# Kernel tuning notes

Hardware: AMD Instinct MI355X
Metric: run time of the kernel (lower is better)

## Reference

```python
import jax, jax.numpy as jnp
import numpy as np

N = 10000  # num_users + num_posts


def gcn_conv(x, edge_index, W, b):
    """PyG-style GCNConv: out = D^-1/2 (A+I) D^-1/2 (x W) + b."""
    h = x @ W  # [N, d]
    src, dst = edge_index[0], edge_index[1]
    loop = jnp.arange(N, dtype=src.dtype)
    src = jnp.concatenate([src, loop])
    dst = jnp.concatenate([dst, loop])
    ones = jnp.ones(src.shape[0], dtype=h.dtype)
    deg = jax.ops.segment_sum(ones, dst, num_segments=N)  # in-degree incl. self-loop
    dinv = jnp.where(deg > 0, jax.lax.rsqrt(deg), 0.0)
    norm = dinv[src] * dinv[dst]  # [E+N]
    msg = h[src] * norm[:, None]  # gather + scale
    out = jax.ops.segment_sum(msg, dst, num_segments=N)  # scatter-add
    return out + b


def setup_inputs() -> dict:
    key = jax.random.key(0)
    k1, k2, k3, k4 = jax.random.split(key, 4)
    E = 320000
    H = 64
    x = jax.random.normal(k1, (N, N), dtype=jnp.float32)
    edge_index = jax.random.randint(k2, (2, E), 0, N, dtype=jnp.int64)
    W1 = jax.random.normal(k3, (N, H), dtype=jnp.float32) / np.sqrt(N)
    b1 = jnp.zeros((H,), dtype=jnp.float32)
    W2 = jax.random.normal(k4, (H, H), dtype=jnp.float32) / np.sqrt(H)
    b2 = jnp.zeros((H,), dtype=jnp.float32)
    return {"x": x, "edge_index": edge_index, "W1": W1, "b1": b1, "W2": W2, "b2": b2}


def reference(x, edge_index, W1, b1, W2, b2):
    h = gcn_conv(x, edge_index, W1, b1)
    h = jax.nn.relu(h)
    return gcn_conv(h, edge_index, W2, b2)
```

## Files before the change

### kernel.cpp

```cpp
#include <hip/hip_runtime.h>
#include <hip/hip_bf16.h>

#define NND 10000
#define HD 64
#define KPAD 10112
#define ROWS 64
#define RBLK 157
#define NCHUNK 3
#define KCHUNK 3456
#define KSTEP 128
#define KHEAD 5632
#define CAP 96
#define ABYTES 32768
#define BBYTES 16384
#define BUFB (ABYTES + BBYTES)

typedef __attribute__((ext_vector_type(8))) short bf16x8;
typedef __attribute__((ext_vector_type(4))) float f32x4;

__device__ __forceinline__ short f2bf(float f) {
    unsigned u = __builtin_bit_cast(unsigned, f);
    u += 0x7FFFu + ((u >> 16) & 1u);
    return (short)(u >> 16);
}

__device__ __forceinline__ void gload16(const void* gp, void* lp) {
    __builtin_amdgcn_global_load_lds(
        (const __attribute__((address_space(1))) unsigned int*)gp,
        (__attribute__((address_space(3))) unsigned int*)lp, 16, 0, 0);
}

__device__ __forceinline__ void gload16nt(const void* gp, void* lp) {
    __builtin_amdgcn_global_load_lds(
        (const __attribute__((address_space(1))) unsigned int*)gp,
        (__attribute__((address_space(3))) unsigned int*)lp, 16, 0, 2);
}

__global__ __launch_bounds__(256) void prep2_kernel(const float* __restrict__ W1,
        int* __restrict__ cnt, float* __restrict__ h, short* __restrict__ w1t) {
    __shared__ float tile[64][65];
    const int t = threadIdx.x;
    const int k0 = blockIdx.x * 64;
    #pragma unroll
    for (int i = 0; i < 16; ++i) {
        int r = i * 4 + (t >> 6);
        int c = t & 63;
        int k = k0 + r;
        tile[r][c] = (k < NND) ? W1[(size_t)k * HD + c] : 0.f;
    }
    __syncthreads();
    #pragma unroll
    for (int i = 0; i < 16; ++i) {
        int c = i * 4 + (t >> 6);
        int k = t & 63;
        if (k0 + k < KPAD)
            w1t[(size_t)c * KPAD + k0 + k] = f2bf(tile[k][c]);
    }
    int tid = blockIdx.x * 256 + t;
    if (tid < NND) cnt[tid] = 0;
    f32x4* h4 = (f32x4*)h;
    f32x4 z = {0.f, 0.f, 0.f, 0.f};
    #pragma unroll
    for (int i = 0; i < 4; ++i) {
        int idx = tid + i * 40448;
        if (idx < NND * HD / 4) h4[idx] = z;
    }
}

__global__ __launch_bounds__(256, 1) void csrgemm1_kernel(const float* __restrict__ x,
        const short* __restrict__ w1t, float* __restrict__ h,
        const int* __restrict__ ei, int* __restrict__ cnt, int* __restrict__ csr, int E) {
    {
        const int stride = RBLK * NCHUNK * 256;
        for (int e = blockIdx.x * 256 + threadIdx.x; e < E; e += stride) {
            int s = ei[e], d = ei[E + e];
            int pos = atomicAdd(&cnt[d], 1);
            if (pos < CAP) csr[d * CAP + pos] = s;
        }
    }
    asm volatile("s_waitcnt vmcnt(0)" ::: "memory");
    __shared__ f32x4 smem4[3 * BUFB / 16];
    char* smem = (char*)smem4;
    const int l = threadIdx.x & 63;
    const int w = threadIdx.x >> 6;
    const int r0 = (blockIdx.x / NCHUNK) * ROWS;
    const int kstart = (blockIdx.x % NCHUNK) * KCHUNK;
    const int kend = min(KPAD, kstart + KCHUNK);
    const int nsteps = (kend - kstart) >> 7;

    const int wr = (w & 1) * 32;
    const int wc = (w >> 1) * 32;
    const int akg = l >> 4;
    const int l15 = l & 15;
    const int l7 = l & 7;

    f32x4 acc[2][2];
    #pragma unroll
    for (int i = 0; i < 2; ++i)
        #pragma unroll
        for (int j = 0; j < 2; ++j) acc[i][j] = f32x4{0.f, 0.f, 0.f, 0.f};

    union AFU { bf16x8 v; __hip_bfloat162 p[4]; };

    auto stage = [&](int buf, int k0) {
        char* sb = smem + buf * BUFB;
        const bool cached = (k0 < KHEAD);
        #pragma unroll
        for (int i = 0; i < 8; ++i) {
            int row = w * 16 + i * 2 + (l >> 5);
            int rg = r0 + row; if (rg >= NND) rg = 0;
            int pl = ((l & 31) >> 1) ^ (row & 7);
            const char* gp = (const char*)x + (size_t)rg * (NND * 4)
                             + (size_t)k0 * 4 + pl * 32 + (l & 1) * 16;
            if (k0 + pl * 8 + (l & 1) * 4 + 3 >= NND)
                gp = (const char*)x;
            if (cached) gload16(gp, sb + w * 8192 + i * 1024);
            else        gload16nt(gp, sb + w * 8192 + i * 1024);
        }
        #pragma unroll
        for (int j = 0; j < 4; ++j) {
            int col = w * 16 + j * 4 + (l >> 4);
            int cl = (l & 15) ^ (col & 7);
            const char* gp = (const char*)w1t + (size_t)col * (KPAD * 2)
                             + (size_t)k0 * 2 + cl * 16;
            gload16(gp, sb + ABYTES + w * 4096 + j * 1024);
        }
    };

    stage(0, kstart);
    if (nsteps > 1) stage(1, kstart + KSTEP);
    for (int t = 0; t < nsteps; ++t) {
        if (t + 1 < nsteps) asm volatile("s_waitcnt vmcnt(12)" ::: "memory");
        else                asm volatile("s_waitcnt vmcnt(0)" ::: "memory");
        __builtin_amdgcn_s_barrier();
        if (t + 2 < nsteps) stage((t + 2) % 3, kstart + (t + 2) * KSTEP);
        const char* sb = smem + (t % 3) * BUFB;
        #pragma unroll
        for (int ks = 0; ks < 4; ++ks) {
            int cp = (ks * 4 + akg) ^ l7;
            #pragma unroll
            for (int rg = 0; rg < 2; ++rg) {
                int arow = wr + rg * 16 + l15;
                const char* ap = sb + arow * 512 + cp * 32;
                f32x4 a0 = *(const f32x4*)ap;
                f32x4 a1 = *(const f32x4*)(ap + 16);
                AFU af;
                af.p[0] = __float22bfloat162_rn(float2{a0[0], a0[1]});
                af.p[1] = __float22bfloat162_rn(float2{a0[2], a0[3]});
                af.p[2] = __float22bfloat162_rn(float2{a1[0], a1[1]});
                af.p[3] = __float22bfloat162_rn(float2{a1[2], a1[3]});
                #pragma unroll
                for (int cg = 0; cg < 2; ++cg) {
                    int col = wc + cg * 16 + l15;
                    bf16x8 b = *(const bf16x8*)(sb + ABYTES + col * 256 + cp * 16);
                    acc[rg][cg] = __builtin_amdgcn_mfma_f32_16x16x32_bf16(af.v, b, acc[rg][cg], 0, 0, 0);
                }
            }
        }
    }
    #pragma unroll
    for (int rg = 0; rg < 2; ++rg) {
        const int crow = r0 + wr + rg * 16 + akg * 4;
        #pragma unroll
        for (int cg = 0; cg < 2; ++cg) {
            const int ccol = wc + cg * 16 + l15;
            #pragma unroll
            for (int j = 0; j < 4; ++j) {
                int row = crow + j;
                if (row < NND)
                    unsafeAtomicAdd(&h[(size_t)row * HD + ccol], acc[rg][cg][j]);
            }
        }
    }
}

__global__ __launch_bounds__(256) void agg1g2_kernel(const float* __restrict__ h,
        const int* __restrict__ csr, const int* __restrict__ cnt,
        const float* __restrict__ b1, const float* __restrict__ W2,
        float* __restrict__ h2) {
    __shared__ float w2s[HD * HD];
    __shared__ float rowbuf[4][HD];
    for (int i = threadIdx.x; i < HD * HD; i += 256) w2s[i] = W2[i];
    const int wave = threadIdx.x >> 6, lane = threadIdx.x & 63;
    const int d = blockIdx.x * 4 + wave;
    const int n = min(cnt[d], CAP);
    const float dd = rsqrtf((float)(n + 1));
    float acc = fmaf(h[(size_t)d * HD + lane], dd * dd, b1[lane]);
    const int* row = csr + d * CAP;
    int j = 0;
    for (; j + 8 <= n; j += 8) {
        int s0 = row[j],   s1 = row[j+1], s2 = row[j+2], s3 = row[j+3];
        int s4 = row[j+4], s5 = row[j+5], s6 = row[j+6], s7 = row[j+7];
        acc = fmaf(h[(size_t)s0 * HD + lane], rsqrtf((float)(cnt[s0] + 1)) * dd, acc);
        acc = fmaf(h[(size_t)s1 * HD + lane], rsqrtf((float)(cnt[s1] + 1)) * dd, acc);
        acc = fmaf(h[(size_t)s2 * HD + lane], rsqrtf((float)(cnt[s2] + 1)) * dd, acc);
        acc = fmaf(h[(size_t)s3 * HD + lane], rsqrtf((float)(cnt[s3] + 1)) * dd, acc);
        acc = fmaf(h[(size_t)s4 * HD + lane], rsqrtf((float)(cnt[s4] + 1)) * dd, acc);
        acc = fmaf(h[(size_t)s5 * HD + lane], rsqrtf((float)(cnt[s5] + 1)) * dd, acc);
        acc = fmaf(h[(size_t)s6 * HD + lane], rsqrtf((float)(cnt[s6] + 1)) * dd, acc);
        acc = fmaf(h[(size_t)s7 * HD + lane], rsqrtf((float)(cnt[s7] + 1)) * dd, acc);
    }
    for (; j < n; ++j) {
        int s0 = row[j];
        acc = fmaf(h[(size_t)s0 * HD + lane], rsqrtf((float)(cnt[s0] + 1)) * dd, acc);
    }
    rowbuf[wave][lane] = fmaxf(acc, 0.f);
    __syncthreads();
    float s = 0.f;
    #pragma unroll
    for (int k = 0; k < HD; ++k)
        s = fmaf(rowbuf[wave][k], w2s[k * HD + lane], s);
    h2[(size_t)d * HD + lane] = s;
}

__global__ __launch_bounds__(256) void agg2_kernel(const float* __restrict__ feat,
        const int* __restrict__ csr, const int* __restrict__ cnt,
        const float* __restrict__ bias, float* __restrict__ out) {
    const int wave = threadIdx.x >> 6, lane = threadIdx.x & 63;
    const int d = blockIdx.x * 4 + wave;
    const int n = min(cnt[d], CAP);
    const float dd = rsqrtf((float)(n + 1));
    float acc = fmaf(feat[(size_t)d * HD + lane], dd * dd, bias[lane]);
    const int* row = csr + d * CAP;
    int j = 0;
    for (; j + 8 <= n; j += 8) {
        int s0 = row[j],   s1 = row[j+1], s2 = row[j+2], s3 = row[j+3];
        int s4 = row[j+4], s5 = row[j+5], s6 = row[j+6], s7 = row[j+7];
        acc = fmaf(feat[(size_t)s0 * HD + lane], rsqrtf((float)(cnt[s0] + 1)) * dd, acc);
        acc = fmaf(feat[(size_t)s1 * HD + lane], rsqrtf((float)(cnt[s1] + 1)) * dd, acc);
        acc = fmaf(feat[(size_t)s2 * HD + lane], rsqrtf((float)(cnt[s2] + 1)) * dd, acc);
        acc = fmaf(feat[(size_t)s3 * HD + lane], rsqrtf((float)(cnt[s3] + 1)) * dd, acc);
        acc = fmaf(feat[(size_t)s4 * HD + lane], rsqrtf((float)(cnt[s4] + 1)) * dd, acc);
        acc = fmaf(feat[(size_t)s5 * HD + lane], rsqrtf((float)(cnt[s5] + 1)) * dd, acc);
        acc = fmaf(feat[(size_t)s6 * HD + lane], rsqrtf((float)(cnt[s6] + 1)) * dd, acc);
        acc = fmaf(feat[(size_t)s7 * HD + lane], rsqrtf((float)(cnt[s7] + 1)) * dd, acc);
    }
    for (; j < n; ++j) {
        int s0 = row[j];
        acc = fmaf(feat[(size_t)s0 * HD + lane], rsqrtf((float)(cnt[s0] + 1)) * dd, acc);
    }
    out[(size_t)d * HD + lane] = acc;
}

extern "C" void kernel_launch(void* const* d_in, const int* in_sizes, int n_in,
                              void* d_out, int out_size, void* d_ws, size_t ws_size,
                              hipStream_t stream) {
    const float* x  = (const float*)d_in[0];
    const int*   ei = (const int*)d_in[1];
    const float* W1 = (const float*)d_in[2];
    const float* b1 = (const float*)d_in[3];
    const float* W2 = (const float*)d_in[4];
    const float* b2 = (const float*)d_in[5];
    float* out = (float*)d_out;
    const int E = in_sizes[1] / 2;

    char* ws = (char*)d_ws;
    int*   cnt  = (int*)(ws);
    float* h    = (float*)(ws + 40000);
    float* h2   = (float*)(ws + 2600000);
    short* w1t  = (short*)(ws + 5160000);
    int*   csr  = (int*)(ws + 6454336);

    prep2_kernel<<<158, 256, 0, stream>>>(W1, cnt, h, w1t);
    csrgemm1_kernel<<<RBLK * NCHUNK, 256, 0, stream>>>(x, w1t, h, ei, cnt, csr, E);
    agg1g2_kernel<<<2500, 256, 0, stream>>>(h, csr, cnt, b1, W2, h2);
    agg2_kernel<<<2500, 256, 0, stream>>>(h2, csr, cnt, b2, out);
}
```

Baseline: 137.1 us.

## Drop split-K in first GEMM, store results directly, overlap CSR build with prefetch

```diff
diff --git a/kernel.cpp b/kernel.cpp
--- a/kernel.cpp
+++ b/kernel.cpp
@@ -6,8 +6,6 @@
 #define KPAD 10112
 #define ROWS 64
 #define RBLK 157
-#define NCHUNK 3
-#define KCHUNK 3456
 #define KSTEP 128
 #define KHEAD 5632
 #define CAP 96
@@ -37,7 +35,7 @@
 }
 
 __global__ __launch_bounds__(256) void prep2_kernel(const float* __restrict__ W1,
-        int* __restrict__ cnt, float* __restrict__ h, short* __restrict__ w1t) {
+        int* __restrict__ cnt, short* __restrict__ w1t) {
     __shared__ float tile[64][65];
     const int t = threadIdx.x;
     const int k0 = blockIdx.x * 64;
@@ -58,35 +56,17 @@
     }
     int tid = blockIdx.x * 256 + t;
     if (tid < NND) cnt[tid] = 0;
-    f32x4* h4 = (f32x4*)h;
-    f32x4 z = {0.f, 0.f, 0.f, 0.f};
-    #pragma unroll
-    for (int i = 0; i < 4; ++i) {
-        int idx = tid + i * 40448;
-        if (idx < NND * HD / 4) h4[idx] = z;
-    }
 }
 
 __global__ __launch_bounds__(256, 1) void csrgemm1_kernel(const float* __restrict__ x,
         const short* __restrict__ w1t, float* __restrict__ h,
         const int* __restrict__ ei, int* __restrict__ cnt, int* __restrict__ csr, int E) {
-    {
-        const int stride = RBLK * NCHUNK * 256;
-        for (int e = blockIdx.x * 256 + threadIdx.x; e < E; e += stride) {
-            int s = ei[e], d = ei[E + e];
-            int pos = atomicAdd(&cnt[d], 1);
-            if (pos < CAP) csr[d * CAP + pos] = s;
-        }
-    }
-    asm volatile("s_waitcnt vmcnt(0)" ::: "memory");
     __shared__ f32x4 smem4[3 * BUFB / 16];
     char* smem = (char*)smem4;
     const int l = threadIdx.x & 63;
     const int w = threadIdx.x >> 6;
-    const int r0 = (blockIdx.x / NCHUNK) * ROWS;
-    const int kstart = (blockIdx.x % NCHUNK) * KCHUNK;
-    const int kend = min(KPAD, kstart + KCHUNK);
-    const int nsteps = (kend - kstart) >> 7;
+    const int r0 = blockIdx.x * ROWS;
+    const int nsteps = KPAD >> 7;
 
     const int wr = (w & 1) * 32;
     const int wc = (w >> 1) * 32;
@@ -127,13 +107,48 @@
         }
     };
 
-    stage(0, kstart);
-    if (nsteps > 1) stage(1, kstart + KSTEP);
+    stage(0, 0);
+    stage(1, KSTEP);
+    {
+        const int tid = blockIdx.x * 256 + threadIdx.x;
+        const int stride8 = RBLK * 256 * 8;
+        for (int base = tid * 8; base < E; base += stride8) {
+            if (base + 8 <= E) {
+                int4 sa = *(const int4*)(ei + base);
+                int4 sb = *(const int4*)(ei + base + 4);
+                int4 da = *(const int4*)(ei + E + base);
+                int4 db = *(const int4*)(ei + E + base + 4);
+                int p0 = atomicAdd(&cnt[da.x], 1);
+                int p1 = atomicAdd(&cnt[da.y], 1);
+                int p2 = atomicAdd(&cnt[da.z], 1);
+                int p3 = atomicAdd(&cnt[da.w], 1);
+                int p4 = atomicAdd(&cnt[db.x], 1);
+                int p5 = atomicAdd(&cnt[db.y], 1);
+                int p6 = atomicAdd(&cnt[db.z], 1);
+                int p7 = atomicAdd(&cnt[db.w], 1);
+                if (p0 < CAP) csr[da.x * CAP + p0] = sa.x;
+                if (p1 < CAP) csr[da.y * CAP + p1] = sa.y;
+                if (p2 < CAP) csr[da.z * CAP + p2] = sa.z;
+                if (p3 < CAP) csr[da.w * CAP + p3] = sa.w;
+                if (p4 < CAP) csr[db.x * CAP + p4] = sb.x;
+                if (p5 < CAP) csr[db.y * CAP + p5] = sb.y;
+                if (p6 < CAP) csr[db.z * CAP + p6] = sb.z;
+                if (p7 < CAP) csr[db.w * CAP + p7] = sb.w;
+            } else {
+                for (int e = base; e < E; ++e) {
+                    int s = ei[e], d = ei[E + e];
+                    int pos = atomicAdd(&cnt[d], 1);
+                    if (pos < CAP) csr[d * CAP + pos] = s;
+                }
+            }
+        }
+    }
+    asm volatile("s_waitcnt vmcnt(0)" ::: "memory");
     for (int t = 0; t < nsteps; ++t) {
         if (t + 1 < nsteps) asm volatile("s_waitcnt vmcnt(12)" ::: "memory");
         else                asm volatile("s_waitcnt vmcnt(0)" ::: "memory");
         __builtin_amdgcn_s_barrier();
-        if (t + 2 < nsteps) stage((t + 2) % 3, kstart + (t + 2) * KSTEP);
+        if (t + 2 < nsteps) stage((t + 2) % 3, (t + 2) * KSTEP);
         const char* sb = smem + (t % 3) * BUFB;
         #pragma unroll
         for (int ks = 0; ks < 4; ++ks) {
@@ -168,7 +183,7 @@
             for (int j = 0; j < 4; ++j) {
                 int row = crow + j;
                 if (row < NND)
-                    unsafeAtomicAdd(&h[(size_t)row * HD + ccol], acc[rg][cg][j]);
+                    h[(size_t)row * HD + ccol] = acc[rg][cg][j];
             }
         }
     }
@@ -261,8 +276,8 @@
     short* w1t  = (short*)(ws + 5160000);
     int*   csr  = (int*)(ws + 6454336);
 
-    prep2_kernel<<<158, 256, 0, stream>>>(W1, cnt, h, w1t);
-    csrgemm1_kernel<<<RBLK * NCHUNK, 256, 0, stream>>>(x, w1t, h, ei, cnt, csr, E);
+    prep2_kernel<<<158, 256, 0, stream>>>(W1, cnt, w1t);
+    csrgemm1_kernel<<<RBLK, 256, 0, stream>>>(x, w1t, h, ei, cnt, csr, E);
     agg1g2_kernel<<<2500, 256, 0, stream>>>(h, csr, cnt, b1, W2, h2);
     agg2_kernel<<<2500, 256, 0, stream>>>(h2, csr, cnt, b2, out);
 }
```

Measured after the change: 158.3 us. 15.5% more time.
